# Optimization experiments

Hardware: AMD Instinct MI355X
Metric: run time of the kernel (lower is better)

## Reference

```python
import jax, jax.numpy as jnp
import numpy as np

LEAKY = 0.1
U, I, D, H, L, E = 100000, 50000, 128, 128, 2, 1600000


def setup_inputs() -> dict:
    key = jax.random.key(0)
    ks = jax.random.split(key, 11)
    s = 1.0 / np.sqrt(D)
    return {
        "uEmbed0": jax.random.normal(ks[0], (U, D), jnp.float32) * s,
        "iEmbed0": jax.random.normal(ks[1], (I, D), jnp.float32) * s,
        "uhyper": jax.random.normal(ks[2], (D, H), jnp.float32) * s,
        "ihyper": jax.random.normal(ks[3], (D, H), jnp.float32) * s,
        "vals": jax.random.uniform(ks[4], (E,), jnp.float32),
        "hgnn_u_W": jax.random.normal(ks[5], (L, 3, H, H), jnp.float32) * (1.0 / np.sqrt(H)),
        "hgnn_i_W": jax.random.normal(ks[6], (L, 3, H, H), jnp.float32) * (1.0 / np.sqrt(H)),
        "gcn_u_W": jax.random.normal(ks[7], (L, D, D), jnp.float32) * s,
        "gcn_i_W": jax.random.normal(ks[8], (L, D, D), jnp.float32) * s,
        "rows": jax.random.randint(ks[9], (E,), 0, U, jnp.int32),
        "cols": jax.random.randint(ks[10], (E,), 0, I, jnp.int32),
    }


def reference(uEmbed0, iEmbed0, uhyper, ihyper, vals, hgnn_u_W, hgnn_i_W, gcn_u_W, gcn_i_W, rows, cols):
    nU, nI = uEmbed0.shape[0], iEmbed0.shape[0]

    def lrelu(x):
        return jax.nn.leaky_relu(x, LEAKY)

    # sparse adjacency (COO) matvecs: adj [nU, nI], adj.T [nI, nU]
    def spmm_u(x):  # adj @ x -> [nU, d]
        return jax.ops.segment_sum(vals[:, None] * x[cols], rows, num_segments=nU)

    def spmm_i(x):  # adj.T @ x -> [nI, d]
        return jax.ops.segment_sum(vals[:, None] * x[rows], cols, num_segments=nI)

    def hgnn(lats, adj, Ws):  # adj: [N, H] dense hyper adjacency, lats: [N, d]
        lat = lrelu(adj.T @ lats)            # [H, d]
        for w in Ws:                         # 3 residual FC blocks on transposed lat
            lat = jax.nn.relu(lat.T @ w).T + lat
        return lrelu(adj @ lat)              # [N, d]

    uuHyper = uEmbed0 @ uhyper  # [nU, H]
    iiHyper = iEmbed0 @ ihyper  # [nI, H]

    ulat, ilat = uEmbed0, iEmbed0
    uSum, iSum = uEmbed0, iEmbed0
    for l in range(hgnn_u_W.shape[0]):
        hU = hgnn(ulat, uuHyper, hgnn_u_W[l])
        hI = hgnn(ilat, iiHyper, hgnn_i_W[l])
        gU = lrelu(jax.nn.relu(spmm_u(ilat) @ gcn_u_W[l]))  # GCNLayer: leaky(relu((adj@lats)@W))
        gI = lrelu(jax.nn.relu(spmm_i(ulat) @ gcn_i_W[l]))
        ulat = gU + hU + ulat
        ilat = gI + hI + ilat
        uSum = uSum + ulat
        iSum = iSum + ilat
    return uSum, iSum
```

## Files before the change

### kernel.cpp

```cpp
#include <hip/hip_runtime.h>
#include <stdint.h>

#define LEAKY 0.1f
typedef unsigned short u16;
typedef unsigned int u32;
typedef short bf16x8 __attribute__((ext_vector_type(8)));
typedef float f32x4 __attribute__((ext_vector_type(4)));

__device__ __forceinline__ float bflo(u32 u){ union{u32 i; float f;} c; c.i = u<<16; return c.f; }
__device__ __forceinline__ float bfhi(u32 u){ union{u32 i; float f;} c; c.i = u & 0xffff0000u; return c.f; }
__device__ __forceinline__ float bf2f(u16 v){ union{u32 i; float f;} c; c.i = ((u32)v)<<16; return c.f; }
__device__ __forceinline__ u16 f2bf(float f){
  union{float f; u32 i;} c; c.f = f;
  u32 r = (c.i + 0x7fffu + ((c.i>>16)&1u)) >> 16;
  return (u16)r;
}
__device__ __forceinline__ u32 pack2(float a, float b){ return (u32)f2bf(a) | ((u32)f2bf(b)<<16); }

__device__ __forceinline__ void load8f(const float* p, float* v){
  const float4* q = (const float4*)p; float4 a = q[0], b = q[1];
  v[0]=a.x;v[1]=a.y;v[2]=a.z;v[3]=a.w;v[4]=b.x;v[5]=b.y;v[6]=b.z;v[7]=b.w;
}
__device__ __forceinline__ void load8h(const u16* p, float* v){
  uint4 u = *(const uint4*)p;
  v[0]=bflo(u.x);v[1]=bfhi(u.x);v[2]=bflo(u.y);v[3]=bfhi(u.y);
  v[4]=bflo(u.z);v[5]=bfhi(u.z);v[6]=bflo(u.w);v[7]=bfhi(u.w);
}
__device__ __forceinline__ void load4f(const float* p, float* v){
  float4 a = *(const float4*)p; v[0]=a.x;v[1]=a.y;v[2]=a.z;v[3]=a.w;
}
__device__ __forceinline__ void load4h(const u16* p, float* v){
  uint2 u = *(const uint2*)p;
  v[0]=bflo(u.x); v[1]=bfhi(u.x); v[2]=bflo(u.y); v[3]=bfhi(u.y);
}
__device__ __forceinline__ void store2bf(u16* p, float a, float b){
  *(u32*)p = pack2(a,b);
}
__device__ __forceinline__ void store4bf(u16* p, float a, float b, float c, float d){
  uint2 t; t.x = pack2(a,b); t.y = pack2(c,d);
  *(uint2*)p = t;
}

__global__ __launch_bounds__(256) void zero_kernel(int* p, int n){
  int i = blockIdx.x*256 + threadIdx.x;
  if (i < n) p[i] = 0;
}

__device__ __forceinline__ void stageWt(const float* __restrict__ W, u16* Wt, int tid){
  const int n = tid & 127, khalf = tid >> 7;
#pragma unroll
  for (int g = 0; g < 16; ++g) {
    int k0 = khalf*64 + g*4;
    float w0 = W[(k0+0)*128 + n];
    float w1 = W[(k0+1)*128 + n];
    float w2 = W[(k0+2)*128 + n];
    float w3 = W[(k0+3)*128 + n];
    uint2 t; t.x = pack2(w0,w1); t.y = pack2(w2,w3);
    *(uint2*)&Wt[n*136 + k0] = t;
  }
}

__device__ __forceinline__ void gemm_core(
    const float* __restrict__ Af, const u16* __restrict__ Ah,
    const float* __restrict__ W, u16* __restrict__ C, int N, int brow,
    u16* Wt, int tid)
{
  stageWt(W, Wt, tid);
  __syncthreads();

  const int w = tid >> 6, lane = tid & 63;
  const int m = lane & 15, quad = lane >> 4;
  const int rowBase = brow*64 + w*16;
  int arow = rowBase + m;
  if (arow >= N) arow = N-1;

  bf16x8 af[4];
  if (Ah) {
#pragma unroll
    for (int kt=0; kt<4; ++kt)
      af[kt] = *(const bf16x8*)(Ah + (size_t)arow*128 + kt*32 + quad*8);
  } else {
#pragma unroll
    for (int kt=0; kt<4; ++kt) {
      float v[8]; load8f(Af + (size_t)arow*128 + kt*32 + quad*8, v);
      bf16x8 t;
#pragma unroll
      for (int j=0;j<8;++j) t[j] = (short)f2bf(v[j]);
      af[kt] = t;
    }
  }

#pragma unroll
  for (int jt=0; jt<8; ++jt) {
    f32x4 acc = {0.f,0.f,0.f,0.f};
#pragma unroll
    for (int kt=0; kt<4; ++kt) {
      bf16x8 bf = *(const bf16x8*)&Wt[(jt*16+m)*136 + kt*32 + quad*8];
      acc = __builtin_amdgcn_mfma_f32_16x16x32_bf16(af[kt], bf, acc, 0, 0, 0);
    }
    const int col = jt*16 + m;
#pragma unroll
    for (int r=0;r<4;++r) {
      int rg = rowBase + quad*4 + r;
      if (rg < N) C[(size_t)rg*128 + col] = f2bf(acc[r]);
    }
  }
}

__global__ __launch_bounds__(256) void gemm128_dual(
    const float* Af1, const u16* Ah1, const float* W1, u16* C1, int N1, int g1,
    const float* Af2, const u16* Ah2, const float* W2, u16* C2, int N2)
{
  __shared__ alignas(16) u16 Wt[128*136];
  const int b = blockIdx.x;
  if (b < g1) gemm_core(Af1, Ah1, W1, C1, N1, b,      Wt, threadIdx.x);
  else        gemm_core(Af2, Ah2, W2, C2, N2, b - g1, Wt, threadIdx.x);
}

__global__ __launch_bounds__(256) void update_dual(
    const u16* T1, const u16* Hy1, const float* W1,
    const float* PF1, const u16* PH1, u16* Po1, float* S1, int N1, int g1,
    const u16* T2, const u16* Hy2, const float* W2,
    const float* PF2, const u16* PH2, u16* Po2, float* S2, int N2, int initS)
{
  __shared__ alignas(16) char shmem[34816];
  u16* Wt = (u16*)shmem;
  float* Gs = (float*)shmem;
  const int tid = threadIdx.x;
  const int b = blockIdx.x;

  const u16* T; const u16* Hy; const float* latW;
  const float* PrevF; const u16* PrevH; u16* Pout; float* S; int N; int brow;
  if (b < g1) { T=T1; Hy=Hy1; latW=W1; PrevF=PF1; PrevH=PH1; Pout=Po1; S=S1; N=N1; brow=b; }
  else        { T=T2; Hy=Hy2; latW=W2; PrevF=PF2; PrevH=PH2; Pout=Po2; S=S2; N=N2; brow=b-g1; }

  stageWt(latW, Wt, tid);
  __syncthreads();

  const int w = tid >> 6, lane = tid & 63;
  const int m = lane & 15, quad = lane >> 4;
  const int rowBase = brow*64;
  int arow = rowBase + w*16 + m;
  if (arow >= N) arow = N-1;

  bf16x8 af[4];
#pragma unroll
  for (int kt=0; kt<4; ++kt)
    af[kt] = *(const bf16x8*)(Hy + (size_t)arow*128 + kt*32 + quad*8);

  f32x4 acc[8];
#pragma unroll
  for (int jt=0; jt<8; ++jt) {
    f32x4 a = {0.f,0.f,0.f,0.f};
#pragma unroll
    for (int kt=0; kt<4; ++kt) {
      bf16x8 bf = *(const bf16x8*)&Wt[(jt*16+m)*136 + kt*32 + quad*8];
      a = __builtin_amdgcn_mfma_f32_16x16x32_bf16(af[kt], bf, a, 0, 0, 0);
    }
    acc[jt] = a;
  }
  __syncthreads();
#pragma unroll
  for (int jt=0; jt<8; ++jt) {
#pragma unroll
    for (int r=0;r<4;++r) {
      float x = acc[jt][r];
      Gs[(w*16 + quad*4 + r)*132 + jt*16 + m] = x > 0.f ? x : LEAKY*x;
    }
  }
  __syncthreads();

  const int c4 = (tid & 31) * 4;
  const int r0 = tid >> 5;
#pragma unroll
  for (int ri=0; ri<8; ++ri) {
    int lr = r0 + ri*8;
    int n = rowBase + lr;
    if (n >= N) continue;
    size_t off = (size_t)n*128 + c4;
    float gv[4]; load4f(&Gs[lr*132 + c4], gv);
    float tv[4], pv[4], ov[4];
    load4h(T + off, tv);
    if (PrevH) load4h(PrevH + off, pv);
    else       load4f(PrevF + off, pv);
#pragma unroll
    for (int cc=0;cc<4;++cc) ov[cc] = gv[cc] + tv[cc] + pv[cc];
    if (Pout)
      store4bf(&Pout[off], ov[0],ov[1],ov[2],ov[3]);
    if (initS) {
      float4 s; s.x=pv[0]+ov[0]; s.y=pv[1]+ov[1]; s.z=pv[2]+ov[2]; s.w=pv[3]+ov[3];
      *(float4*)&S[off] = s;
    } else {
      float4 s = *(const float4*)&S[off];
      s.x += ov[0]; s.y += ov[1]; s.z += ov[2]; s.w += ov[3];
      *(float4*)&S[off] = s;
    }
  }
}

__global__ __launch_bounds__(256) void reduce_kernel(
    const u16* __restrict__ HyU, const u16* __restrict__ HyI,
    const float* __restrict__ LatUf, const u16* __restrict__ LatUh,
    const float* __restrict__ LatIf, const u16* __restrict__ LatIh,
    u16* __restrict__ part, int Nu, int Ni, int nbU)
{
  __shared__ float Hs[32*128];
  __shared__ float Ls[32*128];
  const int b = blockIdx.x;
  const u16* Hy; const float* Lf; const u16* Lh; int N, cstart;
  if (b < nbU) { Hy=HyU; Lf=LatUf; Lh=LatUh; N=Nu; cstart = b*256; }
  else         { Hy=HyI; Lf=LatIf; Lh=LatIh; N=Ni; cstart = (b-nbU)*256; }
  const int cend = (N < cstart+256) ? N : (cstart+256);
  const int tid = threadIdx.x;
  const int ty = tid >> 4, tx = tid & 15;
  const int h0 = ty*8;
  const int dA = tx*4, dB = tx*4+64;
  float acc[8][8];
#pragma unroll
  for (int a=0;a<8;++a)
#pragma unroll
    for (int c=0;c<8;++c) acc[a][c]=0.f;

  for (int t0 = cstart; t0 < cend; t0 += 32) {
#pragma unroll
    for (int j=0;j<2;++j) {
      int e = (j*256+tid)*8;
      int r = e>>7, k = e&127;
      int n = t0 + r;
      float v[8], u[8];
      if (n < cend) {
        load8h(Hy + (size_t)n*128+k, v);
        if (Lh) load8h(Lh + (size_t)n*128+k, u);
        else    load8f(Lf + (size_t)n*128+k, u);
      } else {
        for (int q=0;q<8;++q){v[q]=0.f;u[q]=0.f;}
      }
#pragma unroll
      for (int q=0;q<8;++q){ Hs[r*128+k+q]=v[q]; Ls[r*128+k+q]=u[q]; }
    }
    __syncthreads();
    for (int k=0;k<32;++k) {
      float4 hA = *(const float4*)&Hs[k*128+h0];
      float4 hB = *(const float4*)&Hs[k*128+h0+4];
      float4 lA = *(const float4*)&Ls[k*128+dA];
      float4 lB = *(const float4*)&Ls[k*128+dB];
      float hv[8]; float lv[8];
      hv[0]=hA.x;hv[1]=hA.y;hv[2]=hA.z;hv[3]=hA.w;hv[4]=hB.x;hv[5]=hB.y;hv[6]=hB.z;hv[7]=hB.w;
      lv[0]=lA.x;lv[1]=lA.y;lv[2]=lA.z;lv[3]=lA.w;lv[4]=lB.x;lv[5]=lB.y;lv[6]=lB.z;lv[7]=lB.w;
#pragma unroll
      for (int a=0;a<8;++a)
#pragma unroll
        for (int c=0;c<8;++c)
          acc[a][c] = fmaf(hv[a], lv[c], acc[a][c]);
    }
    __syncthreads();
  }
  u16* pb = part + (size_t)b*16384;
#pragma unroll
  for (int a=0;a<8;++a) {
    int h = h0+a;
    store4bf(&pb[h*128+dA], acc[a][0],acc[a][1],acc[a][2],acc[a][3]);
    store4bf(&pb[h*128+dB], acc[a][4],acc[a][5],acc[a][6],acc[a][7]);
  }
}

#define JS 16
__global__ __launch_bounds__(256) void reduce2a_kernel(
    const u16* __restrict__ part, float* __restrict__ Rp,
    int nbU, int nbI)
{
  const int e = blockIdx.x*256 + threadIdx.x;
  const int side = blockIdx.z;
  const int nb = side ? nbI : nbU;
  const int per = (nb + JS - 1) / JS;
  const int j0 = blockIdx.y * per;
  int j1 = j0 + per; if (j1 > nb) j1 = nb;
  const u16* p = part + (side ? (size_t)nbU*16384 : 0) + e;
  float s = 0.f;
  for (int j=j0; j<j1; ++j) s += bf2f(p[(size_t)j*16384]);
  Rp[((size_t)side*JS + blockIdx.y)*16384 + e] = s;
}

__global__ __launch_bounds__(256) void reduce2b_kernel(
    const float* __restrict__ Rp, float* __restrict__ Ru, float* __restrict__ Ri)
{
  const int e = blockIdx.x*256 + threadIdx.x;
  const int side = blockIdx.y;
  const float* p = Rp + (size_t)side*JS*16384 + e;
  float s = 0.f;
#pragma unroll
  for (int j=0; j<JS; ++j) s += p[(size_t)j*16384];
  if (side) Ri[e] = s; else Ru[e] = s;
}

__global__ __launch_bounds__(128) void fc_kernel(
    const float* __restrict__ Ru, const float* __restrict__ Ri,
    const float* __restrict__ W3u, const float* __restrict__ W3i,
    float* __restrict__ latU, float* __restrict__ latI)
{
  __shared__ float cur[128];
  const int h = threadIdx.x;
  const int d = blockIdx.x;
  const int side = blockIdx.y;
  const float* R  = side ? Ri  : Ru;
  const float* W3 = side ? W3i : W3u;
  float* lat      = side ? latI : latU;
  float x = R[h*128 + d];
  cur[h] = x > 0.f ? x : LEAKY*x;
  __syncthreads();
  for (int s=0;s<3;++s) {
    const float* w = W3 + s*16384 + h;
    float val = 0.f;
#pragma unroll 8
    for (int hp=0; hp<128; ++hp) val = fmaf(cur[hp], w[hp*128], val);
    val = (val > 0.f ? val : 0.f) + cur[h];
    __syncthreads();
    cur[h] = val;
    __syncthreads();
  }
  lat[h*128+d] = cur[h];
}

__global__ __launch_bounds__(256) void spmm_kernel(
    const uint2* __restrict__ csr, const int* __restrict__ rowptr,
    const u16* __restrict__ Y, u16* __restrict__ T, int N, int Ncol, int E)
{
  const int lane = threadIdx.x & 63;
  const int row = blockIdx.x*4 + (threadIdx.x >> 6);
  if (row >= N) return;
  int e  = rowptr[row];
  int e1 = rowptr[row+1];
  if (e < 0) e = 0;
  if (e > E) e = E;
  if (e1 < e) e1 = e;
  if (e1 > E) e1 = E;
  const u32 cmax = (u32)(Ncol - 1);
  float a0=0.f, a1=0.f;
  const int c2 = lane*2;
  for (; e+4 <= e1; e += 4) {
    uint2 p0 = csr[e], p1 = csr[e+1], p2 = csr[e+2], p3 = csr[e+3];
    u32 i0 = p0.x < cmax ? p0.x : cmax;
    u32 i1 = p1.x < cmax ? p1.x : cmax;
    u32 i2 = p2.x < cmax ? p2.x : cmax;
    u32 i3 = p3.x < cmax ? p3.x : cmax;
    u32 y0 = *(const u32*)&Y[(size_t)i0*128 + c2];
    u32 y1 = *(const u32*)&Y[(size_t)i1*128 + c2];
    u32 y2 = *(const u32*)&Y[(size_t)i2*128 + c2];
    u32 y3 = *(const u32*)&Y[(size_t)i3*128 + c2];
    float v0 = __uint_as_float(p0.y), v1 = __uint_as_float(p1.y);
    float v2 = __uint_as_float(p2.y), v3 = __uint_as_float(p3.y);
    a0 = fmaf(v0, bflo(y0), a0); a1 = fmaf(v0, bfhi(y0), a1);
    a0 = fmaf(v1, bflo(y1), a0); a1 = fmaf(v1, bfhi(y1), a1);
    a0 = fmaf(v2, bflo(y2), a0); a1 = fmaf(v2, bfhi(y2), a1);
    a0 = fmaf(v3, bflo(y3), a0); a1 = fmaf(v3, bfhi(y3), a1);
  }
  for (; e < e1; ++e) {
    uint2 p0 = csr[e];
    u32 i0 = p0.x < cmax ? p0.x : cmax;
    u32 y0 = *(const u32*)&Y[(size_t)i0*128 + c2];
    float v0 = __uint_as_float(p0.y);
    a0 = fmaf(v0, bflo(y0), a0); a1 = fmaf(v0, bfhi(y0), a1);
  }
  store2bf(&T[(size_t)row*128 + c2], a0 > 0.f ? a0 : 0.f, a1 > 0.f ? a1 : 0.f);
}

#define HCB 32768
#define HWORDS (HCB/2)
#define HS  64
__global__ __launch_bounds__(256) void hist_part_kernel(
    const int* __restrict__ rows, const int* __restrict__ cols,
    u32* __restrict__ part, int E, int cU)
{
  __shared__ alignas(16) u32 h[HWORDS];
  const int c = blockIdx.x, s = blockIdx.y;
  const int* key = (c < cU) ? rows : cols;
  const u32 lo = (u32)((c < cU ? c : c - cU) * HCB);
  {
    uint4 z; z.x=0; z.y=0; z.z=0; z.w=0;
    uint4* h4 = (uint4*)h;
    for (int i = threadIdx.x; i < HWORDS/4; i += 256) h4[i] = z;
  }
  __syncthreads();
  int per = (E + HS - 1) / HS;
  per = (per + 3) & ~3;
  const int e0 = s*per;
  const int e1 = (E < e0+per) ? E : (e0+per);
  if (e0 < e1) {
    const int4* kp = (const int4*)(key + e0);
    const int nv = (e1 - e0) >> 2;
    for (int i = threadIdx.x; i < nv; i += 256) {
      int4 kv = kp[i];
      u32 k0=(u32)kv.x-lo, k1=(u32)kv.y-lo, k2=(u32)kv.z-lo, k3=(u32)kv.w-lo;
      if (k0 < (u32)HCB) atomicAdd(&h[k0>>1], 1u << ((k0&1)<<4));
      if (k1 < (u32)HCB) atomicAdd(&h[k1>>1], 1u << ((k1&1)<<4));
      if (k2 < (u32)HCB) atomicAdd(&h[k2>>1], 1u << ((k2&1)<<4));
      if (k3 < (u32)HCB) atomicAdd(&h[k3>>1], 1u << ((k3&1)<<4));
    }
    for (int e = e0 + (nv<<2) + threadIdx.x; e < e1; e += 256) {
      u32 k = (u32)key[e] - lo;
      if (k < (u32)HCB) atomicAdd(&h[k>>1], 1u << ((k&1)<<4));
    }
  }
  __syncthreads();
  uint4* dst = (uint4*)(part + (size_t)(c*HS + s) * HWORDS);
  const uint4* h4 = (const uint4*)h;
  for (int i = threadIdx.x; i < HWORDS/4; i += 256) dst[i] = h4[i];
}

__global__ __launch_bounds__(256) void scan_local_kernel(
    const u32* __restrict__ part,
    int* rpU, int* rpI, int* bsU, int* bsI, int Nu, int Ni, int cU)
{
  const int side = blockIdx.y;
  const int Nn = side ? Ni : Nu;
  int* rp = side ? rpI : rpU;
  int* bs = side ? bsI : bsU;
  const int nb = (Nn + 4095) >> 12;
  if ((int)blockIdx.x >= nb) return;
  __shared__ int sa[256], sb[256];
  const int tid = threadIdx.x;
  const int base = blockIdx.x*4096 + tid*16;
  int v[16];
#pragma unroll
  for (int q=0;q<16;++q) v[q]=0;
  {
    const int gc = (side ? cU : 0) + (base >> 15);
    const int w0 = (base & (HCB-1)) >> 1;
    const u32* ps = part + (size_t)gc*HS*HWORDS + w0;
    for (int s=0; s<HS; ++s) {
      const uint4* pw = (const uint4*)(ps + (size_t)s*HWORDS);
      uint4 a = pw[0], b = pw[1];
      v[0]+= (int)(a.x&0xffffu); v[1]+= (int)(a.x>>16);
      v[2]+= (int)(a.y&0xffffu); v[3]+= (int)(a.y>>16);
      v[4]+= (int)(a.z&0xffffu); v[5]+= (int)(a.z>>16);
      v[6]+= (int)(a.w&0xffffu); v[7]+= (int)(a.w>>16);
      v[8]+= (int)(b.x&0xffffu); v[9]+= (int)(b.x>>16);
      v[10]+=(int)(b.y&0xffffu); v[11]+=(int)(b.y>>16);
      v[12]+=(int)(b.z&0xffffu); v[13]+=(int)(b.z>>16);
      v[14]+=(int)(b.w&0xffffu); v[15]+=(int)(b.w>>16);
    }
  }
  int sum = 0;
#pragma unroll
  for (int q=0;q<16;++q) sum += v[q];
  sa[tid] = sum; __syncthreads();
  int* src = sa; int* dst = sb;
  for (int off=1; off<256; off<<=1) {
    int x = src[tid] + ((tid>=off) ? src[tid-off] : 0);
    dst[tid] = x;
    __syncthreads();
    int* t = src; src = dst; dst = t;
  }
  const int incl = src[tid];
  int run = incl - sum;
#pragma unroll
  for (int q=0;q<16;++q){ int idx=base+q; if (idx<Nn) rp[idx]=run; run+=v[q]; }
  if (tid==255) bs[blockIdx.x] = incl;
}

__global__ void scan_blocks_kernel(int* bsU, int* bsI, int* rpU, int* rpI, int Nu, int Ni)
{
  if (threadIdx.x != 0) return;
  const int side = blockIdx.y;
  int* bs = side?bsI:bsU; int* rp = side?rpI:rpU;
  const int Nn = side?Ni:Nu;
  const int nb = (Nn+4095)>>12;
  int run = 0;
  for (int b=0;b<nb;++b){ int t=bs[b]; bs[b]=run; run+=t; }
  rp[Nn] = run;
}

__global__ __launch_bounds__(256) void scan_add_kernel(
    const int* bsU, const int* bsI, int* rpU, int* rpI, int Nu, int Ni)
{
  const int side = blockIdx.y;
  const int Nn = side?Ni:Nu;
  const int* bs = side?bsI:bsU;
  int* rp = side?rpI:rpU;
  const int nb = (Nn+4095)>>12;
  if ((int)blockIdx.x >= nb) return;
  const int add = bs[blockIdx.x];
  const int base = blockIdx.x*4096 + threadIdx.x*16;
#pragma unroll
  for (int q=0;q<16;++q){ int idx=base+q; if (idx<Nn) rp[idx]+=add; }
}

__global__ __launch_bounds__(256) void scatter_kernel(
    const int* __restrict__ rows, const int* __restrict__ cols, const float* __restrict__ vals,
    const int* __restrict__ rpU, const int* __restrict__ rpI,
    int* curU, int* curI, uint2* csrU, uint2* csrI, int E, int Nu, int Ni,
    int u0, int u1, int i0w, int i1w)
{
  int e = blockIdx.x*256 + threadIdx.x;
  if (e >= E) return;
  int r = rows[e], c = cols[e];
  if ((unsigned)r < (unsigned)Nu && (unsigned)c < (unsigned)Ni) {
    u32 vb = __float_as_uint(vals[e]);
    if (r >= u0 && r < u1) {
      int su = rpU[r] + atomicAdd(&curU[r], 1);
      if ((unsigned)su < (unsigned)E) { uint2 t; t.x=(u32)c; t.y=vb; csrU[su]=t; }
    }
    if (c >= i0w && c < i1w) {
      int si = rpI[c] + atomicAdd(&curI[c], 1);
      if ((unsigned)si < (unsigned)E) { uint2 t; t.x=(u32)r; t.y=vb; csrI[si]=t; }
    }
  }
}

extern "C" void kernel_launch(void* const* d_in, const int* in_sizes, int n_in,
                              void* d_out, int out_size, void* d_ws, size_t ws_size,
                              hipStream_t stream)
{
  const float* uE     = (const float*)d_in[0];
  const float* iE     = (const float*)d_in[1];
  const float* uhyper = (const float*)d_in[2];
  const float* ihyper = (const float*)d_in[3];
  const float* vals   = (const float*)d_in[4];
  const float* WhU    = (const float*)d_in[5];
  const float* WhI    = (const float*)d_in[6];
  const float* WgU    = (const float*)d_in[7];
  const float* WgI    = (const float*)d_in[8];
  const int*   rows   = (const int*)d_in[9];
  const int*   cols   = (const int*)d_in[10];
  const int U = in_sizes[0]/128;
  const int I = in_sizes[1]/128;
  const int E = in_sizes[4];
  const int L = in_sizes[7]/(128*128);
  (void)n_in; (void)out_size;

  float* Su = (float*)d_out;
  float* Si = Su + (size_t)U*128;

  char* base0 = (char*)d_ws;
  u16* uuH; u16* iiH; u16* PU; u16* PI; u16* YU; u16* TU; u16* pool3;
  uint2* csrU; uint2* csrI; int* rpU; int* rpI; int* cntU; int* cntI;
  int* bsU; int* bsI; float* Ru; float* Ri; float* latU; float* latI; float* Rp;
  {
    size_t off = 0;
    #define ALLOC(var, type, bytes) var = (type)(base0 + off); off = (off + (bytes) + 255) & ~(size_t)255;
    ALLOC(uuH,  u16*, (size_t)U*128*2)
    ALLOC(iiH,  u16*, (size_t)I*128*2)
    ALLOC(PU,   u16*, (size_t)U*128*2)
    ALLOC(PI,   u16*, (size_t)I*128*2)
    ALLOC(YU,   u16*, (size_t)U*128*2)
    ALLOC(TU,   u16*, (size_t)U*128*2)
    ALLOC(pool3,u16*, (size_t)I*128*2)
    ALLOC(csrU, uint2*, (size_t)E*8)
    ALLOC(csrI, uint2*, (size_t)E*8)
    ALLOC(rpU,  int*, (size_t)(U+1)*4)
    ALLOC(rpI,  int*, (size_t)(I+1)*4)
    ALLOC(cntU, int*, (size_t)U*4)
    ALLOC(cntI, int*, (size_t)I*4)
    ALLOC(bsU,  int*, 64*4)
    ALLOC(bsI,  int*, 64*4)
    ALLOC(Ru,   float*, 16384*4)
    ALLOC(Ri,   float*, 16384*4)
    ALLOC(latU, float*, 16384*4)
    ALLOC(latI, float*, 16384*4)
    ALLOC(Rp,   float*, (size_t)2*JS*16384*4)
    #undef ALLOC
    if (off > ws_size) return;
  }
  const int cntN = (int)(((size_t)((char*)bsU - (char*)cntU)) / 4);

  const int nbU = (U+4095)>>12, nbI = (I+4095)>>12;
  const int nbMax = nbU > nbI ? nbU : nbI;
  const int rbU = (U+255)>>8, rbI = (I+255)>>8;
  const int gU = (U+63)/64, gI = (I+63)/64;
  const int cU = (U + HCB-1)/HCB, cI = (I + HCB-1)/HCB;

  u32* hpart = (u32*)csrU;

  hist_part_kernel<<<dim3(cU+cI, HS), 256, 0, stream>>>(rows, cols, hpart, E, cU);
  scan_local_kernel<<<dim3(nbMax,2), 256, 0, stream>>>(hpart,rpU,rpI,bsU,bsI,U,I,cU);
  scan_blocks_kernel<<<dim3(1,2), 64, 0, stream>>>(bsU,bsI,rpU,rpI,U,I);
  scan_add_kernel<<<dim3(nbMax,2), 256, 0, stream>>>(bsU,bsI,rpU,rpI,U,I);
  zero_kernel<<<(cntN+255)/256, 256, 0, stream>>>(cntU, cntN);
  for (int wnd = 0; wnd < 4; ++wnd) {
    int u0 = (int)(((long long)wnd   * U) / 4);
    int u1 = (int)(((long long)(wnd+1) * U) / 4);
    int i0w = (int)(((long long)wnd   * I) / 4);
    int i1w = (int)(((long long)(wnd+1) * I) / 4);
    scatter_kernel<<<(E+255)/256, 256, 0, stream>>>(
        rows, cols, vals, rpU, rpI, cntU, cntI, csrU, csrI, E, U, I,
        u0, u1, i0w, i1w);
  }

  gemm128_dual<<<gU+gI, 256, 0, stream>>>(uE, (const u16*)0, uhyper, uuH, U, gU,
                                          iE, (const u16*)0, ihyper, iiH, I);

  for (int l=0; l<L; ++l) {
    const float* wgu = WgU + (size_t)l*16384;
    const float* wgi = WgI + (size_t)l*16384;
    const float* whu = WhU + (size_t)l*3*16384;
    const float* whi = WhI + (size_t)l*3*16384;
    const bool last = (l == L-1);
    if (l == 0) {
      gemm128_dual<<<gI+gU, 256, 0, stream>>>(iE, (const u16*)0, wgu, pool3, I, gI,
                                              uE, (const u16*)0, wgi, YU, U);
      spmm_kernel<<<(U+3)/4, 256, 0, stream>>>(csrU, rpU, pool3, TU, U, I, E);
      spmm_kernel<<<(I+3)/4, 256, 0, stream>>>(csrI, rpI, YU, pool3, I, U, E);
      reduce_kernel<<<rbU+rbI, 256, 0, stream>>>(uuH,iiH, uE,(const u16*)0, iE,(const u16*)0, YU,U,I,rbU);
      reduce2a_kernel<<<dim3(64,JS,2), 256, 0, stream>>>(YU, Rp, rbU, rbI);
      reduce2b_kernel<<<dim3(64,2), 256, 0, stream>>>(Rp, Ru, Ri);
      fc_kernel<<<dim3(128,2), 128, 0, stream>>>(Ru,Ri,whu,whi,latU,latI);
      update_dual<<<gU+gI, 256, 0, stream>>>(
          TU,    uuH, latU, uE, (const u16*)0, PU, Su, U, gU,
          pool3, iiH, latI, iE, (const u16*)0, PI, Si, I, 1);
    } else {
      gemm128_dual<<<gI+gU, 256, 0, stream>>>((const float*)0, PI, wgu, pool3, I, gI,
                                              (const float*)0, PU, wgi, YU, U);
      spmm_kernel<<<(U+3)/4, 256, 0, stream>>>(csrU, rpU, pool3, TU, U, I, E);
      spmm_kernel<<<(I+3)/4, 256, 0, stream>>>(csrI, rpI, YU, pool3, I, U, E);
      reduce_kernel<<<rbU+rbI, 256, 0, stream>>>(uuH,iiH, (const float*)0,PU, (const float*)0,PI, YU,U,I,rbU);
      reduce2a_kernel<<<dim3(64,JS,2), 256, 0, stream>>>(YU, Rp, rbU, rbI);
      reduce2b_kernel<<<dim3(64,2), 256, 0, stream>>>(Rp, Ru, Ri);
      fc_kernel<<<dim3(128,2), 128, 0, stream>>>(Ru,Ri,whu,whi,latU,latI);
      update_dual<<<gU+gI, 256, 0, stream>>>(
          TU,    uuH, latU, (const float*)0, PU, last?(u16*)0:PU, Su, U, gU,
          pool3, iiH, latI, (const float*)0, PI, last?(u16*)0:PI, Si, I, 0);
    }
  }
}
```

Before: 1.029 ms.

## Use bf16 MFMA for hyper-adjacency reduction instead of scalar FMA

Rewrites the reduce kernel that computes adj^T @ lats partials to stage the tiles as transposed bf16 in padded shared memory and run 16x16x32 bf16 MFMA instructions instead of an 8x8 per-thread fp32 FMA outer product. The aim is to cut the ALU cost of this reduction by moving it onto the matrix cores. In exchange, fp32 latents are rounded to bf16 before the multiply, the transposed LDS writes become scattered 16-bit stores, and the output stores become narrow, uncoalesced 16-bit writes.

```diff
diff --git a/kernel.cpp b/kernel.cpp
--- a/kernel.cpp
+++ b/kernel.cpp
@@ -198,69 +198,82 @@
   }
 }
 
+#define RPAD 40
 __global__ __launch_bounds__(256) void reduce_kernel(
     const u16* __restrict__ HyU, const u16* __restrict__ HyI,
     const float* __restrict__ LatUf, const u16* __restrict__ LatUh,
     const float* __restrict__ LatIf, const u16* __restrict__ LatIh,
     u16* __restrict__ part, int Nu, int Ni, int nbU)
 {
-  __shared__ float Hs[32*128];
-  __shared__ float Ls[32*128];
+  __shared__ alignas(16) u16 HsT[128*RPAD];
+  __shared__ alignas(16) u16 LsT[128*RPAD];
   const int b = blockIdx.x;
   const u16* Hy; const float* Lf; const u16* Lh; int N, cstart;
   if (b < nbU) { Hy=HyU; Lf=LatUf; Lh=LatUh; N=Nu; cstart = b*256; }
   else         { Hy=HyI; Lf=LatIf; Lh=LatIh; N=Ni; cstart = (b-nbU)*256; }
   const int cend = (N < cstart+256) ? N : (cstart+256);
   const int tid = threadIdx.x;
-  const int ty = tid >> 4, tx = tid & 15;
-  const int h0 = ty*8;
-  const int dA = tx*4, dB = tx*4+64;
-  float acc[8][8];
-#pragma unroll
-  for (int a=0;a<8;++a)
-#pragma unroll
-    for (int c=0;c<8;++c) acc[a][c]=0.f;
+  const int w = tid >> 6, lane = tid & 63;
+  const int m = lane & 15, quad = lane >> 4;
+
+  f32x4 acc[2][8];
+#pragma unroll
+  for (int a=0;a<2;++a)
+#pragma unroll
+    for (int c=0;c<8;++c) { acc[a][c][0]=0.f; acc[a][c][1]=0.f; acc[a][c][2]=0.f; acc[a][c][3]=0.f; }
 
   for (int t0 = cstart; t0 < cend; t0 += 32) {
 #pragma unroll
-    for (int j=0;j<2;++j) {
-      int e = (j*256+tid)*8;
-      int r = e>>7, k = e&127;
-      int n = t0 + r;
-      float v[8], u[8];
-      if (n < cend) {
-        load8h(Hy + (size_t)n*128+k, v);
-        if (Lh) load8h(Lh + (size_t)n*128+k, u);
-        else    load8f(Lf + (size_t)n*128+k, u);
-      } else {
-        for (int q=0;q<8;++q){v[q]=0.f;u[q]=0.f;}
+    for (int it=0; it<2; ++it) {
+      const int idx = it*256 + tid;
+      const int n = idx & 31, h0 = (idx >> 5) * 8;
+      const int row = t0 + n;
+      u32 ax=0, ay=0, az=0, aw=0, lx=0, ly=0, lz=0, lw=0;
+      if (row < cend) {
+        uint4 uh = *(const uint4*)(Hy + (size_t)row*128 + h0);
+        ax=uh.x; ay=uh.y; az=uh.z; aw=uh.w;
+        if (Lh) {
+          uint4 ul = *(const uint4*)(Lh + (size_t)row*128 + h0);
+          lx=ul.x; ly=ul.y; lz=ul.z; lw=ul.w;
+        } else {
+          float v[8]; load8f(Lf + (size_t)row*128 + h0, v);
+          lx = pack2(v[0],v[1]); ly = pack2(v[2],v[3]);
+          lz = pack2(v[4],v[5]); lw = pack2(v[6],v[7]);
+        }
       }
-#pragma unroll
-      for (int q=0;q<8;++q){ Hs[r*128+k+q]=v[q]; Ls[r*128+k+q]=u[q]; }
+      u16* hp = &HsT[h0*RPAD + n];
+      hp[0*RPAD]=(u16)ax; hp[1*RPAD]=(u16)(ax>>16);
+      hp[2*RPAD]=(u16)ay; hp[3*RPAD]=(u16)(ay>>16);
+      hp[4*RPAD]=(u16)az; hp[5*RPAD]=(u16)(az>>16);
+      hp[6*RPAD]=(u16)aw; hp[7*RPAD]=(u16)(aw>>16);
+      u16* lp = &LsT[h0*RPAD + n];
+      lp[0*RPAD]=(u16)lx; lp[1*RPAD]=(u16)(lx>>16);
+      lp[2*RPAD]=(u16)ly; lp[3*RPAD]=(u16)(ly>>16);
+      lp[4*RPAD]=(u16)lz; lp[5*RPAD]=(u16)(lz>>16);
+      lp[6*RPAD]=(u16)lw; lp[7*RPAD]=(u16)(lw>>16);
     }
     __syncthreads();
-    for (int k=0;k<32;++k) {
-      float4 hA = *(const float4*)&Hs[k*128+h0];
-      float4 hB = *(const float4*)&Hs[k*128+h0+4];
-      float4 lA = *(const float4*)&Ls[k*128+dA];
-      float4 lB = *(const float4*)&Ls[k*128+dB];
-      float hv[8]; float lv[8];
-      hv[0]=hA.x;hv[1]=hA.y;hv[2]=hA.z;hv[3]=hA.w;hv[4]=hB.x;hv[5]=hB.y;hv[6]=hB.z;hv[7]=hB.w;
-      lv[0]=lA.x;lv[1]=lA.y;lv[2]=lA.z;lv[3]=lA.w;lv[4]=lB.x;lv[5]=lB.y;lv[6]=lB.z;lv[7]=lB.w;
-#pragma unroll
-      for (int a=0;a<8;++a)
-#pragma unroll
-        for (int c=0;c<8;++c)
-          acc[a][c] = fmaf(hv[a], lv[c], acc[a][c]);
+    bf16x8 a0 = *(const bf16x8*)&HsT[(w*32 +      m)*RPAD + quad*8];
+    bf16x8 a1 = *(const bf16x8*)&HsT[(w*32 + 16 + m)*RPAD + quad*8];
+#pragma unroll
+    for (int td=0; td<8; ++td) {
+      bf16x8 bfr = *(const bf16x8*)&LsT[(td*16 + m)*RPAD + quad*8];
+      acc[0][td] = __builtin_amdgcn_mfma_f32_16x16x32_bf16(a0, bfr, acc[0][td], 0, 0, 0);
+      acc[1][td] = __builtin_amdgcn_mfma_f32_16x16x32_bf16(a1, bfr, acc[1][td], 0, 0, 0);
     }
     __syncthreads();
   }
   u16* pb = part + (size_t)b*16384;
 #pragma unroll
-  for (int a=0;a<8;++a) {
-    int h = h0+a;
-    store4bf(&pb[h*128+dA], acc[a][0],acc[a][1],acc[a][2],acc[a][3]);
-    store4bf(&pb[h*128+dB], acc[a][4],acc[a][5],acc[a][6],acc[a][7]);
+  for (int th=0; th<2; ++th) {
+    const int h = w*32 + th*16 + quad*4;
+#pragma unroll
+    for (int td=0; td<8; ++td) {
+      const int d = td*16 + m;
+#pragma unroll
+      for (int r=0;r<4;++r)
+        pb[(size_t)(h+r)*128 + d] = f2bf(acc[th][td][r]);
+    }
   }
 }
 
```

Result: faster. 928.8 us (-9.8%).
